# Optimization experiments

Measured on AMD Instinct MI355X. Metric: run time of the kernel, lower is better.

The kernel has to match this reference:

```python
import jax, jax.numpy as jnp
import numpy as np

L = 4          # num_layers
D = 512        # gconv_dim == tlayer_dim
HG, CG = 8, 64 # gconv heads, head dim (D//8)
HT, CT = 4, 128  # tlayer heads, head dim
FF = 4 * D
G, NPG = 128, 256
N = G * NPG
E = N * 16
AF, AV = 9, 64   # atom features / vocab
BF, BV = 3, 8    # bond features / vocab
OUT = 128
SCALE = 0.02


def setup_inputs() -> dict:
    key = jax.random.key(0)
    ks = iter(jax.random.split(key, 64))
    rn = lambda shape: (jax.random.normal(next(ks), shape, dtype=jnp.float32) * SCALE)
    inp = {}
    # float params (stacked over layers)
    inp['atom_emb'] = rn((AF, AV, D))
    inp['bond_emb'] = rn((BF, BV, D))
    for nm in ['gq_w', 'gk_w', 'gv_w', 'ge_w', 'gskip_w', 'mid_w']:
        inp[nm] = rn((L, D, D))
    for nm in ['gq_b', 'gk_b', 'gv_b', 'gskip_b', 'mid_b']:
        inp[nm] = rn((L, D))
    inp['mid_g'] = jnp.ones((L, D), jnp.float32)
    inp['mid_bt'] = jnp.zeros((L, D), jnp.float32)
    for nm in ['tq_w', 'tk_w', 'tv_w', 'to_w']:
        inp[nm] = rn((L, D, D))
    for nm in ['tq_b', 'tk_b', 'tv_b', 'to_b']:
        inp[nm] = rn((L, D))
    inp['ln1_g'] = jnp.ones((L, D), jnp.float32)
    inp['ln1_b'] = jnp.zeros((L, D), jnp.float32)
    inp['f1_w'] = rn((L, D, FF))
    inp['f1_b'] = rn((L, FF))
    inp['f2_w'] = rn((L, FF, D))
    inp['f2_b'] = rn((L, D))
    inp['ln2_g'] = jnp.ones((L, D), jnp.float32)
    inp['ln2_b'] = jnp.zeros((L, D), jnp.float32)
    inp['out_w'] = rn((D, OUT))
    inp['out_b'] = rn((OUT,))
    # int inputs
    inp['x'] = jax.random.randint(next(ks), (N, AF), 0, AV, dtype=jnp.int32)
    inp['edge_attr'] = jax.random.randint(next(ks), (E, BF), 0, BV, dtype=jnp.int32)
    # intra-graph edges: random offsets within each graph
    gid = jax.random.randint(next(ks), (E,), 0, G, dtype=jnp.int32)
    src = gid * NPG + jax.random.randint(next(ks), (E,), 0, NPG, dtype=jnp.int32)
    dst = gid * NPG + jax.random.randint(next(ks), (E,), 0, NPG, dtype=jnp.int32)
    inp['edge_index'] = jnp.stack([src, dst])
    inp['batch'] = jnp.repeat(jnp.arange(G, dtype=jnp.int32), NPG)
    return inp


def _ln(x, g, b, eps=1e-5):
    mu = x.mean(-1, keepdims=True)
    var = ((x - mu) ** 2).mean(-1, keepdims=True)
    return (x - mu) * jax.lax.rsqrt(var + eps) * g + b


def _forward(atom_emb, bond_emb, gq_w, gq_b, gk_w, gk_b, gv_w, gv_b, ge_w,
             gskip_w, gskip_b, mid_w, mid_b, mid_g, mid_bt,
             tq_w, tq_b, tk_w, tk_b, tv_w, tv_b, to_w, to_b,
             ln1_g, ln1_b, f1_w, f1_b, f2_w, f2_b, ln2_g, ln2_b,
             out_w, out_b, x, edge_index, edge_attr, batch):
    # encoders: sum of per-feature embeddings (OGB AtomEncoder/BondEncoder)
    h = atom_emb[jnp.arange(AF)[None, :], x].sum(1)          # [N, D]
    e_attr = bond_emb[jnp.arange(BF)[None, :], edge_attr].sum(1)  # [E, D]
    src, dst = edge_index[0], edge_index[1]

    for i in range(L):
        # --- TransformerConv (PyG): edge-conditioned multi-head graph attention
        q = (h @ gq_w[i] + gq_b[i]).reshape(N, HG, CG)
        k = (h @ gk_w[i] + gk_b[i]).reshape(N, HG, CG)
        v = (h @ gv_w[i] + gv_b[i]).reshape(N, HG, CG)
        ee = (e_attr @ ge_w[i]).reshape(E, HG, CG)           # lin_edge (no bias)
        ke = k[src] + ee
        ve = v[src] + ee
        logits = (q[dst] * ke).sum(-1) / np.sqrt(CG)          # [E, HG]
        m = jax.ops.segment_max(logits, dst, num_segments=N)
        p = jnp.exp(logits - m[dst])
        denom = jax.ops.segment_sum(p, dst, num_segments=N) + 1e-16
        alpha = p / denom[dst]
        agg = jax.ops.segment_sum(alpha[..., None] * ve, dst, num_segments=N)
        h = agg.reshape(N, D) + h @ gskip_w[i] + gskip_b[i]   # root skip
        # --- middle Linear + LayerNorm + ReLU
        h = jax.nn.relu(_ln(h @ mid_w[i] + mid_b[i], mid_g[i], mid_bt[i]))

    xg = h.reshape(G, NPG, D)
    for i in range(L):
        # --- transformer encoder layer, dense attention within each graph
        q = (xg @ tq_w[i] + tq_b[i]).reshape(G, NPG, HT, CT)
        k = (xg @ tk_w[i] + tk_b[i]).reshape(G, NPG, HT, CT)
        v = (xg @ tv_w[i] + tv_b[i]).reshape(G, NPG, HT, CT)
        attn = jax.nn.softmax(jnp.einsum('gqhc,gkhc->ghqk', q, k) / np.sqrt(CT), axis=-1)
        o = jnp.einsum('ghqk,gkhc->gqhc', attn, v).reshape(G, NPG, D)
        xg = _ln(xg + (o @ to_w[i] + to_b[i]), ln1_g[i], ln1_b[i])
        ff = jax.nn.relu(xg @ f1_w[i] + f1_b[i]) @ f2_w[i] + f2_b[i]
        xg = _ln(xg + ff, ln2_g[i], ln2_b[i])

    # mean readout over nodes per graph (segment mean via batch)
    hflat = xg.reshape(N, D)
    cnt = jax.ops.segment_sum(jnp.ones((N,), hflat.dtype), batch, num_segments=G)
    pooled = jax.ops.segment_sum(hflat, batch, num_segments=G) / cnt[:, None]
    return pooled @ out_w + out_b                              # [G, OUT]


def reference(atom_emb, bond_emb, gq_w, gq_b, gk_w, gk_b, gv_w, gv_b, ge_w,
              gskip_w, gskip_b, mid_w, mid_b, mid_g, mid_bt,
              tq_w, tq_b, tk_w, tk_b, tv_w, tv_b, to_w, to_b,
              ln1_g, ln1_b, f1_w, f1_b, f2_w, f2_b, ln2_g, ln2_b,
              out_w, out_b, x, edge_index, edge_attr, batch):
    return _forward(atom_emb, bond_emb, gq_w, gq_b, gk_w, gk_b, gv_w, gv_b, ge_w,
                    gskip_w, gskip_b, mid_w, mid_b, mid_g, mid_bt,
                    tq_w, tq_b, tk_w, tk_b, tv_w, tv_b, to_w, to_b,
                    ln1_g, ln1_b, f1_w, f1_b, f2_w, f2_b, ln2_g, ln2_b,
                    out_w, out_b, x, edge_index, edge_attr, batch)
```

## Files before the change

### kernel.cpp

```cpp
#include <hip/hip_runtime.h>
#include <hip/hip_bf16.h>
#include <math.h>

#define N_NODES 32768
#define DIM     512
#define NE      524288
#define NL      4
#define NG      128
#define NPG_    256
#define HG_     8
#define CG_     64
#define HT_     4
#define CT_     128
#define FF_     2048
#define AF_     9
#define AV_     64
#define BV_     8
#define OUTD    128

typedef unsigned short u16;
typedef __attribute__((ext_vector_type(8))) short bhalf8;
typedef __attribute__((ext_vector_type(4))) float floatx4;
typedef __attribute__((ext_vector_type(8))) unsigned short u16x8;
typedef __attribute__((ext_vector_type(4))) unsigned short u16x4;

__device__ __forceinline__ u16 f2bf(float f) {
  union { float f; unsigned u; } x; x.f = f;
  unsigned r = x.u + 0x7fffu + ((x.u >> 16) & 1u);
  return (u16)(r >> 16);
}
__device__ __forceinline__ float bf2f(u16 u) {
  union { unsigned u; float f; } x; x.u = ((unsigned)u) << 16; return x.f;
}

#define GL2LDS(gp, lp) __builtin_amdgcn_global_load_lds( \
    (const __attribute__((address_space(1))) unsigned int*)(gp), \
    (__attribute__((address_space(3))) unsigned int*)(lp), 16, 0, 0)

__global__ __launch_bounds__(128) void atom_enc_kernel(
    const float* __restrict__ emb, const int* __restrict__ x, u16* __restrict__ hb) {
  int n = blockIdx.x;
  int d4 = threadIdx.x;
  const int* xr = x + n * AF_;
  float4 acc = {0.f, 0.f, 0.f, 0.f};
#pragma unroll
  for (int f = 0; f < AF_; ++f) {
    int idx = xr[f];
    const float4 v = *(const float4*)&emb[((size_t)(f * AV_ + idx)) * DIM + 4 * d4];
    acc.x += v.x; acc.y += v.y; acc.z += v.z; acc.w += v.w;
  }
  u16x4 o;
  o[0] = f2bf(acc.x); o[1] = f2bf(acc.y); o[2] = f2bf(acc.z); o[3] = f2bf(acc.w);
  *(u16x4*)&hb[(size_t)n * DIM + 4 * d4] = o;
}

__global__ __launch_bounds__(512) void bemb_proj_kernel(
    const float* __restrict__ bond_emb, const float* __restrict__ gew, u16* __restrict__ tab) {
  __shared__ float red[8][64];
  int r = blockIdx.x;
  int col = (threadIdx.x & 63) + blockIdx.y * 64;
  int kp = threadIdx.x >> 6;
  const float* a = bond_emb + (size_t)r * DIM + kp * 64;
  const float* w = gew + (size_t)kp * 64 * DIM + col;
  float acc = 0.f;
#pragma unroll 8
  for (int kx = 0; kx < 64; ++kx)
    acc += a[kx] * w[(size_t)kx * DIM];
  red[kp][threadIdx.x & 63] = acc;
  __syncthreads();
  if (threadIdx.x < 64) {
    float s = 0.f;
#pragma unroll
    for (int p = 0; p < 8; ++p) s += red[p][threadIdx.x];
    tab[(size_t)r * DIM + col] = f2bf(s);
  }
}

__global__ __launch_bounds__(256) void wcvt_kernel(
    const float* __restrict__ W, u16* __restrict__ Wt, int K, int N, size_t ostride) {
  __shared__ float t[32][33];
  const size_t mi = (size_t)blockIdx.z * K * N;
  const size_t mo = (size_t)blockIdx.z * ostride;
  int k0 = blockIdx.y * 32, n0 = blockIdx.x * 32;
  int tx = threadIdx.x & 31, ty = threadIdx.x >> 5;
#pragma unroll
  for (int i = 0; i < 32; i += 8)
    t[ty + i][tx] = W[mi + (size_t)(k0 + ty + i) * N + n0 + tx];
  __syncthreads();
#pragma unroll
  for (int i = 0; i < 32; i += 8)
    Wt[mo + (size_t)(n0 + ty + i) * K + k0 + tx] = f2bf(t[tx][ty + i]);
}

__global__ __launch_bounds__(256) void gemm_mfma_kernel(
    const u16* __restrict__ A, const u16* __restrict__ Bt,
    const float* __restrict__ bias, const float* __restrict__ bias1,
    const float* __restrict__ bias2, const float* __restrict__ bias3,
    float* __restrict__ Cf, u16* __restrict__ Cb,
    u16* __restrict__ R1, u16* __restrict__ R2, float* __restrict__ R3f,
    int K, int Nout, int relu, int bf16out, int vtout, int route) {
  __shared__ __align__(16) u16 As[4096];
  __shared__ __align__(16) u16 Bs[4096];
  const int tid = threadIdx.x;
  const int wave = tid >> 6, lane = tid & 63;
  const int bm = blockIdx.y * 128, bn = blockIdx.x * 128;
  const int wr = wave >> 1, wc = wave & 1;

  const size_t rowA = (size_t)bm + (tid >> 2);
  const size_t rowB = (size_t)bn + (tid >> 2);
  const int gofs = (tid & 3) * 8;
  const u16* pA = A + rowA * K + gofs;
  const u16* pB = Bt + rowB * K + gofs;
  u16* lA0 = &As[wave * 512];
  u16* lB0 = &Bs[wave * 512];
  const size_t skip64 = (size_t)64 * K;

  floatx4 acc[4][4] = {};
  const int r = lane & 15, kg = lane >> 4;
  const int aoff = (wr * 64 + r) * 32 + kg * 8;
  const int boff = (wc * 64 + r) * 32 + kg * 8;

  for (int k0 = 0; k0 < K; k0 += 32) {
    GL2LDS(pA + k0, lA0);
    GL2LDS(pA + skip64 + k0, lA0 + 2048);
    GL2LDS(pB + k0, lB0);
    GL2LDS(pB + skip64 + k0, lB0 + 2048);
    __syncthreads();
    bhalf8 af[4], bg[4];
#pragma unroll
    for (int mi = 0; mi < 4; ++mi) af[mi] = *(const bhalf8*)&As[aoff + mi * 512];
#pragma unroll
    for (int ni = 0; ni < 4; ++ni) bg[ni] = *(const bhalf8*)&Bs[boff + ni * 512];
#pragma unroll
    for (int mi = 0; mi < 4; ++mi)
#pragma unroll
      for (int ni = 0; ni < 4; ++ni)
        acc[mi][ni] = __builtin_amdgcn_mfma_f32_16x16x32_bf16(af[mi], bg[ni], acc[mi][ni], 0, 0, 0);
    __syncthreads();
  }

  const int rb = (lane >> 4) * 4;
  const int cc = lane & 15;
  const int seg = (route != 0) ? (bn >> 9) : 0;
  const float* bp = bias;
  if (route != 0) {
    if (seg == 1) bp = bias1;
    else if (seg == 2) bp = bias2;
    else if (seg == 3) bp = bias3;
  }
#pragma unroll
  for (int mi = 0; mi < 4; ++mi) {
#pragma unroll
    for (int ni = 0; ni < 4; ++ni) {
      int gr0 = bm + wr * 64 + mi * 16 + rb;
      int gc = bn + wc * 64 + ni * 16 + cc;
      int c = (route != 0) ? (gc & 511) : gc;
      float bv = bp[c];
#pragma unroll
      for (int reg = 0; reg < 4; ++reg) {
        int gr = gr0 + reg;
        float v = acc[mi][ni][reg] + bv;
        if (relu) v = fmaxf(v, 0.f);
        if (route == 1) {
          size_t idx = (size_t)gr * 512 + c;
          if (seg == 0)      Cb[idx] = f2bf(v);
          else if (seg == 1) R1[idx] = f2bf(v);
          else if (seg == 2) R2[idx] = f2bf(v);
          else               R3f[idx] = v;
        } else if (route == 2) {
          if (seg == 0)      Cb[(size_t)gr * 512 + c] = f2bf(v);
          else if (seg == 1) R1[(size_t)gr * 512 + c] = f2bf(v);
          else               R2[((size_t)(gr >> 8) * DIM + c) * NPG_ + (gr & 255)] = f2bf(v);
        } else if (vtout) {
          Cb[((size_t)(gr >> 8) * DIM + gc) * NPG_ + (gr & 255)] = f2bf(v);
        } else if (bf16out) {
          Cb[(size_t)gr * Nout + gc] = f2bf(v);
        } else {
          Cf[(size_t)gr * Nout + gc] = v;
        }
      }
    }
  }
}

__global__ __launch_bounds__(256) void attn_s_mfma_kernel(
    const u16* __restrict__ q, const u16* __restrict__ k, u16* __restrict__ S, int zbase) {
  __shared__ __align__(16) u16 As[4096];
  __shared__ __align__(16) u16 Bs[4096];
  const int tid = threadIdx.x;
  const int wave = tid >> 6, lane = tid & 63;
  const int zl = blockIdx.z, z = zbase + zl, g = z >> 2, hh = z & 3;
  const int bm = blockIdx.y * 128, bn = blockIdx.x * 128;
  const int wr = wave >> 1, wc = wave & 1;
  const u16* qg = q + (size_t)g * NPG_ * DIM + hh * CT_;
  const u16* kg2 = k + (size_t)g * NPG_ * DIM + hh * CT_;
  const u16* pA = qg + (size_t)(bm + (tid >> 2)) * DIM + (tid & 3) * 8;
  const u16* pB = kg2 + (size_t)(bn + (tid >> 2)) * DIM + (tid & 3) * 8;
  u16* lA0 = &As[wave * 512];
  u16* lB0 = &Bs[wave * 512];
  const size_t skip64 = (size_t)64 * DIM;
  floatx4 acc[4][4] = {};
  const int r = lane & 15, kg_ = lane >> 4;
  const int aoff = (wr * 64 + r) * 32 + kg_ * 8;
  const int boff = (wc * 64 + r) * 32 + kg_ * 8;
  for (int k0 = 0; k0 < CT_; k0 += 32) {
    GL2LDS(pA + k0, lA0);
    GL2LDS(pA + skip64 + k0, lA0 + 2048);
    GL2LDS(pB + k0, lB0);
    GL2LDS(pB + skip64 + k0, lB0 + 2048);
    __syncthreads();
    bhalf8 af[4], bg[4];
#pragma unroll
    for (int mi = 0; mi < 4; ++mi) af[mi] = *(const bhalf8*)&As[aoff + mi * 512];
#pragma unroll
    for (int ni = 0; ni < 4; ++ni) bg[ni] = *(const bhalf8*)&Bs[boff + ni * 512];
#pragma unroll
    for (int mi = 0; mi < 4; ++mi)
#pragma unroll
      for (int ni = 0; ni < 4; ++ni)
        acc[mi][ni] = __builtin_amdgcn_mfma_f32_16x16x32_bf16(af[mi], bg[ni], acc[mi][ni], 0, 0, 0);
    __syncthreads();
  }
  const float sc = 0.08838834764831845f;
  u16* C = S + (size_t)zl * NPG_ * NPG_;
  const int rb = (lane >> 4) * 4, cc = lane & 15;
#pragma unroll
  for (int mi = 0; mi < 4; ++mi)
#pragma unroll
    for (int ni = 0; ni < 4; ++ni) {
      int gr = bm + wr * 64 + mi * 16 + rb;
      int gc = bn + wc * 64 + ni * 16 + cc;
#pragma unroll
      for (int reg = 0; reg < 4; ++reg)
        C[(size_t)(gr + reg) * NPG_ + gc] = f2bf(acc[mi][ni][reg] * sc);
    }
}

__global__ __launch_bounds__(256) void softmax256_kernel(u16* __restrict__ SP) {
  size_t row = (size_t)blockIdx.x * 4 + (threadIdx.x >> 6);
  int lane = threadIdx.x & 63;
  u16* r = SP + row * NPG_;
  u16x4 v = *(u16x4*)&r[lane * 4];
  float x0 = bf2f(v[0]), x1 = bf2f(v[1]), x2 = bf2f(v[2]), x3 = bf2f(v[3]);
  float m = fmaxf(fmaxf(x0, x1), fmaxf(x2, x3));
#pragma unroll
  for (int off = 32; off; off >>= 1) m = fmaxf(m, __shfl_xor(m, off));
  x0 = expf(x0 - m); x1 = expf(x1 - m); x2 = expf(x2 - m); x3 = expf(x3 - m);
  float s = x0 + x1 + x2 + x3;
#pragma unroll
  for (int off = 32; off; off >>= 1) s += __shfl_xor(s, off);
  float inv = 1.0f / s;
  u16x4 o;
  o[0] = f2bf(x0 * inv); o[1] = f2bf(x1 * inv);
  o[2] = f2bf(x2 * inv); o[3] = f2bf(x3 * inv);
  *(u16x4*)&r[lane * 4] = o;
}

__global__ __launch_bounds__(256) void attn_o_mfma_kernel(
    const u16* __restrict__ P, const u16* __restrict__ vt, u16* __restrict__ O, int zbase) {
  __shared__ __align__(16) u16 As[4096];
  __shared__ __align__(16) u16 Bs[4096];
  const int tid = threadIdx.x;
  const int wave = tid >> 6, lane = tid & 63;
  const int zl = blockIdx.z, z = zbase + zl, g = z >> 2, hh = z & 3;
  const int bm = blockIdx.y * 128;
  const int wr = wave >> 1, wc = wave & 1;
  const u16* A = P + (size_t)zl * NPG_ * NPG_;
  const u16* Bt = vt + ((size_t)g * DIM + hh * CT_) * NPG_;
  const u16* pA = A + (size_t)(bm + (tid >> 2)) * NPG_ + (tid & 3) * 8;
  const u16* pB = Bt + (size_t)(tid >> 2) * NPG_ + (tid & 3) * 8;
  u16* lA0 = &As[wave * 512];
  u16* lB0 = &Bs[wave * 512];
  const size_t skip64 = (size_t)64 * NPG_;
  floatx4 acc[4][4] = {};
  const int r = lane & 15, kg_ = lane >> 4;
  const int aoff = (wr * 64 + r) * 32 + kg_ * 8;
  const int boff = (wc * 64 + r) * 32 + kg_ * 8;
  for (int k0 = 0; k0 < NPG_; k0 += 32) {
    GL2LDS(pA + k0, lA0);
    GL2LDS(pA + skip64 + k0, lA0 + 2048);
    GL2LDS(pB + k0, lB0);
    GL2LDS(pB + skip64 + k0, lB0 + 2048);
    __syncthreads();
    bhalf8 af[4], bg[4];
#pragma unroll
    for (int mi = 0; mi < 4; ++mi) af[mi] = *(const bhalf8*)&As[aoff + mi * 512];
#pragma unroll
    for (int ni = 0; ni < 4; ++ni) bg[ni] = *(const bhalf8*)&Bs[boff + ni * 512];
#pragma unroll
    for (int mi = 0; mi < 4; ++mi)
#pragma unroll
      for (int ni = 0; ni < 4; ++ni)
        acc[mi][ni] = __builtin_amdgcn_mfma_f32_16x16x32_bf16(af[mi], bg[ni], acc[mi][ni], 0, 0, 0);
    __syncthreads();
  }
  u16* C = O + ((size_t)g * NPG_) * DIM + hh * CT_;
  const int rb = (lane >> 4) * 4, cc = lane & 15;
#pragma unroll
  for (int mi = 0; mi < 4; ++mi)
#pragma unroll
    for (int ni = 0; ni < 4; ++ni) {
      int gr = bm + wr * 64 + mi * 16 + rb;
      int gc = wc * 64 + ni * 16 + cc;
#pragma unroll
      for (int reg = 0; reg < 4; ++reg)
        C[(size_t)(gr + reg) * DIM + gc] = f2bf(acc[mi][ni][reg]);
    }
}

__global__ __launch_bounds__(256) void gemm_bias_kernel(
    const float* __restrict__ A, const float* __restrict__ W,
    const float* __restrict__ bias, float* __restrict__ C,
    int M, int K, int Nout, int relu) {
  __shared__ float As[16][65];
  __shared__ float Bs[16][64];
  const int bm = blockIdx.y * 64;
  const int bn = blockIdx.x * 64;
  const int tid = threadIdx.x;
  const int tx = tid & 15, ty = tid >> 4;
  float acc[4][4] = {};
  for (int k0 = 0; k0 < K; k0 += 16) {
    {
      int row = tid >> 2;
      int kq = (tid & 3) << 2;
      float4 a = *(const float4*)&A[(size_t)(bm + row) * K + k0 + kq];
      As[kq + 0][row] = a.x; As[kq + 1][row] = a.y; As[kq + 2][row] = a.z; As[kq + 3][row] = a.w;
    }
    {
      int krow = tid >> 4;
      int cq = (tid & 15) << 2;
      *(float4*)&Bs[krow][cq] = *(const float4*)&W[(size_t)(k0 + krow) * Nout + bn + cq];
    }
    __syncthreads();
#pragma unroll
    for (int kk = 0; kk < 16; ++kk) {
      float a[4];
#pragma unroll
      for (int i = 0; i < 4; ++i) a[i] = As[kk][ty * 4 + i];
      float4 b4 = *(const float4*)&Bs[kk][tx * 4];
      float b[4] = {b4.x, b4.y, b4.z, b4.w};
#pragma unroll
      for (int i = 0; i < 4; ++i)
#pragma unroll
        for (int j = 0; j < 4; ++j) acc[i][j] = fmaf(a[i], b[j], acc[i][j]);
    }
    __syncthreads();
  }
  float4 bv = *(const float4*)&bias[bn + tx * 4];
#pragma unroll
  for (int i = 0; i < 4; ++i) {
    int row = bm + ty * 4 + i;
    float4 o;
    o.x = acc[i][0] + bv.x; o.y = acc[i][1] + bv.y;
    o.z = acc[i][2] + bv.z; o.w = acc[i][3] + bv.w;
    if (relu) {
      o.x = fmaxf(o.x, 0.f); o.y = fmaxf(o.y, 0.f);
      o.z = fmaxf(o.z, 0.f); o.w = fmaxf(o.w, 0.f);
    }
    *(float4*)&C[(size_t)row * Nout + bn + tx * 4] = o;
  }
}

__global__ __launch_bounds__(256) void deg_count_kernel(const int* __restrict__ ei, int* __restrict__ deg) {
  int e = blockIdx.x * 256 + threadIdx.x;
  atomicAdd(&deg[ei[NE + e]], 1);
}

__global__ __launch_bounds__(1024) void scan_kernel(const int* __restrict__ deg, int* __restrict__ rp) {
  __shared__ int sums[1024];
  int t = threadIdx.x;
  int base = t * 32;
  int local[32];
  int s = 0;
#pragma unroll
  for (int i = 0; i < 32; ++i) { local[i] = s; s += deg[base + i]; }
  sums[t] = s;
  __syncthreads();
  for (int off = 1; off < 1024; off <<= 1) {
    int other = (t >= off) ? sums[t - off] : 0;
    __syncthreads();
    sums[t] += other;
    __syncthreads();
  }
  int chunk_off = sums[t] - s;
#pragma unroll
  for (int i = 0; i < 32; ++i) rp[base + i] = chunk_off + local[i];
  if (t == 1023) rp[N_NODES] = sums[1023];
}

__global__ __launch_bounds__(256) void scatter_kernel(
    const int* __restrict__ ei, const int* __restrict__ rp,
    int* __restrict__ cur, int* __restrict__ csr) {
  int e = blockIdx.x * 256 + threadIdx.x;
  int d = ei[NE + e];
  int pos = atomicAdd(&cur[d], 1);
  csr[rp[d] + pos] = e;
}

#define CHUNK 128
__global__ __launch_bounds__(512) void edge_agg_kernel(
    const u16* __restrict__ q, const u16* __restrict__ k, const u16* __restrict__ v,
    const u16* __restrict__ tab, const float* __restrict__ skip,
    const int* __restrict__ ei, const int* __restrict__ ea,
    const int* __restrict__ rp, const int* __restrict__ csr, u16* __restrict__ hnew) {
  int n = blockIdx.x;
  int d = threadIdx.x;
  int hh = d >> 6;
  int lane = d & 63;
  int start = rp[n];
  int deg = rp[n + 1] - start;
  __shared__ int s_src[CHUNK];
  __shared__ int s_ea[CHUNK];
  __shared__ float s_p[CHUNK * HG_];
  __shared__ float s_q[DIM];
  __shared__ float s_w[24 * HG_];
  __shared__ float s_max[HG_];
  __shared__ float s_resc[HG_];
  s_q[d] = bf2f(q[(size_t)n * DIM + d]);
  if (d < 24 * HG_) s_w[d] = 0.f;
  if (d < HG_) s_max[d] = -3.0e38f;
  float accum = 0.f, den = 0.f;
  for (int c0 = 0; c0 < deg; c0 += CHUNK) {
    int cnt = min(CHUNK, deg - c0);
    __syncthreads();
    if (d < cnt) {
      int eid = csr[start + c0 + d];
      s_src[d] = ei[eid];
      s_ea[d] = ea[eid * 3] | (ea[eid * 3 + 1] << 8) | (ea[eid * 3 + 2] << 16);
    }
    __syncthreads();
    for (int j = hh; j < cnt; j += 8) {
      int srcn = s_src[j];
      int eap = s_ea[j];
      const u16x8 kv = *(const u16x8*)&k[(size_t)srcn * DIM + lane * 8];
      const size_t to = (size_t)lane * 8;
      const u16x8 e0 = *(const u16x8*)&tab[(size_t)(eap & 0xff) * DIM + to];
      const u16x8 e1 = *(const u16x8*)&tab[(size_t)(8 + ((eap >> 8) & 0xff)) * DIM + to];
      const u16x8 e2 = *(const u16x8*)&tab[(size_t)(16 + (eap >> 16)) * DIM + to];
      float acc = 0.f;
#pragma unroll
      for (int jj = 0; jj < 8; ++jj) {
        float ee = bf2f(e0[jj]) + bf2f(e1[jj]) + bf2f(e2[jj]);
        acc += s_q[lane * 8 + jj] * (bf2f(kv[jj]) + ee);
      }
      acc += __shfl_xor(acc, 1);
      acc += __shfl_xor(acc, 2);
      acc += __shfl_xor(acc, 4);
      if ((lane & 7) == 0) s_p[j * HG_ + (lane >> 3)] = acc * 0.125f;
    }
    __syncthreads();
    float cm = -3.0e38f;
    for (int j = lane; j < cnt; j += 64)
      cm = fmaxf(cm, s_p[j * HG_ + hh]);
#pragma unroll
    for (int off = 32; off; off >>= 1) cm = fmaxf(cm, __shfl_xor(cm, off));
    if (lane == 0) {
      float om = s_max[hh];
      float nm = fmaxf(om, cm);
      s_resc[hh] = (nm > om) ? expf(om - nm) : 1.0f;
      s_max[hh] = nm;
    }
    __syncthreads();
    float rsc = s_resc[hh];
    accum *= rsc;
    den *= rsc;
    if (d < 24 * HG_) s_w[d] *= s_resc[d & 7];
    __syncthreads();
    for (int jh = d; jh < cnt * HG_; jh += 512) {
      int h2 = jh & 7;
      float p = expf(s_p[jh] - s_max[h2]);
      s_p[jh] = p;
      int eap = s_ea[jh >> 3];
      atomicAdd(&s_w[(eap & 0xff) * HG_ + h2], p);
      atomicAdd(&s_w[(8 + ((eap >> 8) & 0xff)) * HG_ + h2], p);
      atomicAdd(&s_w[(16 + (eap >> 16)) * HG_ + h2], p);
    }
    __syncthreads();
    for (int j = 0; j < cnt; ++j) {
      float p = s_p[j * HG_ + hh];
      den += p;
      accum = fmaf(p, bf2f(v[(size_t)s_src[j] * DIM + d]), accum);
    }
  }
  __syncthreads();
#pragma unroll
  for (int r2 = 0; r2 < 24; ++r2)
    accum = fmaf(s_w[r2 * HG_ + hh], bf2f(tab[(size_t)r2 * DIM + d]), accum);
  size_t o = (size_t)n * DIM + d;
  hnew[o] = f2bf(accum / (den + 1e-16f) + skip[o]);
}

__global__ __launch_bounds__(256) void ln_kernel(
    const float* __restrict__ in, const u16* __restrict__ resid,
    const float* __restrict__ g, const float* __restrict__ b,
    u16* __restrict__ outb, int relu) {
  int row = blockIdx.x * 4 + (threadIdx.x >> 6);
  int lane = threadIdx.x & 63;
  size_t base = (size_t)row * DIM + lane * 8;
  float x[8];
  {
    float4 v0 = *(const float4*)&in[base];
    float4 v1 = *(const float4*)&in[base + 4];
    x[0] = v0.x; x[1] = v0.y; x[2] = v0.z; x[3] = v0.w;
    x[4] = v1.x; x[5] = v1.y; x[6] = v1.z; x[7] = v1.w;
  }
  if (resid) {
    u16x8 rv = *(const u16x8*)&resid[base];
#pragma unroll
    for (int i = 0; i < 8; ++i) x[i] += bf2f(rv[i]);
  }
  float s = 0.f;
#pragma unroll
  for (int i = 0; i < 8; ++i) s += x[i];
#pragma unroll
  for (int off = 32; off; off >>= 1) s += __shfl_xor(s, off);
  float mu = s * (1.0f / DIM);
  float vs = 0.f;
#pragma unroll
  for (int i = 0; i < 8; ++i) { float t = x[i] - mu; vs += t * t; }
#pragma unroll
  for (int off = 32; off; off >>= 1) vs += __shfl_xor(vs, off);
  float rstd = 1.0f / sqrtf(vs * (1.0f / DIM) + 1e-5f);
  float4 g0 = *(const float4*)&g[lane * 8];
  float4 g1 = *(const float4*)&g[lane * 8 + 4];
  float4 b0 = *(const float4*)&b[lane * 8];
  float4 b1 = *(const float4*)&b[lane * 8 + 4];
  float gg[8] = {g0.x, g0.y, g0.z, g0.w, g1.x, g1.y, g1.z, g1.w};
  float bb[8] = {b0.x, b0.y, b0.z, b0.w, b1.x, b1.y, b1.z, b1.w};
  u16x8 ob;
#pragma unroll
  for (int i = 0; i < 8; ++i) {
    float y = (x[i] - mu) * rstd * gg[i] + bb[i];
    if (relu) y = fmaxf(y, 0.f);
    ob[i] = f2bf(y);
  }
  *(u16x8*)&outb[base] = ob;
}

__global__ __launch_bounds__(512) void pool_kernel(const u16* __restrict__ xg, float* __restrict__ pooled) {
  int g = blockIdx.x;
  int d = threadIdx.x;
  float acc = 0.f;
  for (int p = 0; p < NPG_; ++p) acc += bf2f(xg[((size_t)g * NPG_ + p) * DIM + d]);
  pooled[(size_t)g * DIM + d] = acc * (1.0f / NPG_);
}

extern "C" void kernel_launch(void* const* d_in, const int* in_sizes, int n_in,
                              void* d_out, int out_size, void* d_ws, size_t ws_size,
                              hipStream_t stream) {
  const float* atom_emb = (const float*)d_in[0];
  const float* bond_emb = (const float*)d_in[1];
  const float* gq_w = (const float*)d_in[2];
  const float* gk_w = (const float*)d_in[3];
  const float* gv_w = (const float*)d_in[4];
  const float* ge_w = (const float*)d_in[5];
  const float* gskip_w = (const float*)d_in[6];
  const float* mid_w = (const float*)d_in[7];
  const float* gq_b = (const float*)d_in[8];
  const float* gk_b = (const float*)d_in[9];
  const float* gv_b = (const float*)d_in[10];
  const float* gskip_b = (const float*)d_in[11];
  const float* mid_b = (const float*)d_in[12];
  const float* mid_g = (const float*)d_in[13];
  const float* mid_bt = (const float*)d_in[14];
  const float* tq_w = (const float*)d_in[15];
  const float* tk_w = (const float*)d_in[16];
  const float* tv_w = (const float*)d_in[17];
  const float* to_w = (const float*)d_in[18];
  const float* tq_b = (const float*)d_in[19];
  const float* tk_b = (const float*)d_in[20];
  const float* tv_b = (const float*)d_in[21];
  const float* to_b = (const float*)d_in[22];
  const float* ln1_g = (const float*)d_in[23];
  const float* ln1_b = (const float*)d_in[24];
  const float* f1_w = (const float*)d_in[25];
  const float* f1_b = (const float*)d_in[26];
  const float* f2_w = (const float*)d_in[27];
  const float* f2_b = (const float*)d_in[28];
  const float* ln2_g = (const float*)d_in[29];
  const float* ln2_b = (const float*)d_in[30];
  const float* out_w = (const float*)d_in[31];
  const float* out_b = (const float*)d_in[32];
  const int* x = (const int*)d_in[33];
  const int* ea = (const int*)d_in[34];
  const int* ei = (const int*)d_in[35];

  char* wbase = (char*)d_ws;
  size_t woff = 0;
  auto ALLOC = [&](size_t bytes) -> void* {
    void* r = wbase + woff;
    woff += (bytes + 255) & ~(size_t)255;
    return r;
  };
  const size_t ND = (size_t)N_NODES * DIM * sizeof(float);
  const size_t NDH = (size_t)N_NODES * DIM * sizeof(u16);
  u16*   wt     = (u16*)ALLOC((size_t)17825792 * sizeof(u16));
  u16*   hb     = (u16*)ALLOC(NDH);
  u16*   Abuf   = (u16*)ALLOC(NDH);
  u16*   Bbuf   = (u16*)ALLOC(NDH);
  u16*   Cbuf   = (u16*)ALLOC(NDH);
  float* E      = (float*)ALLOC(ND);
  u16*   U      = (u16*)ALLOC((size_t)16777216);
  u16*   tab    = (u16*)ALLOC(24 * DIM * sizeof(u16));
  float* pooled = (float*)ALLOC((size_t)NG * DIM * sizeof(float));
  int* deg      = (int*)ALLOC(N_NODES * sizeof(int));
  int* cur      = (int*)ALLOC(N_NODES * sizeof(int));
  int* rp       = (int*)ALLOC((N_NODES + 1) * sizeof(int));
  int* csr      = (int*)ALLOC((size_t)NE * sizeof(int));
  (void)ws_size; (void)in_sizes; (void)n_in; (void)out_size;

  const size_t DD = (size_t)DIM * DIM;
  u16* gfT  = wt;
  u16* midT = wt + 16 * DD;
  u16* tfT  = wt + 20 * DD;
  u16* toT  = wt + 32 * DD;
  u16* f1T  = wt + 36 * DD;
  u16* f2T  = wt + 52 * DD;

  auto wcvt = [&](const float* W, u16* Wt, int K, int N, int L2, size_t ostride) {
    dim3 grid(N / 32, K / 32, L2);
    wcvt_kernel<<<grid, 256, 0, stream>>>(W, Wt, K, N, ostride);
  };
  auto mgemm = [&](const u16* A_, const u16* Bt_, const float* bias_,
                   float* Cf_, u16* Cb_, int M_, int K_, int Nout_,
                   int relu_, int bf16o_, int vtout_) {
    dim3 grid(Nout_ / 128, M_ / 128);
    gemm_mfma_kernel<<<grid, 256, 0, stream>>>(A_, Bt_, bias_, nullptr, nullptr, nullptr,
                                               Cf_, Cb_, nullptr, nullptr, nullptr,
                                               K_, Nout_, relu_, bf16o_, vtout_, 0);
  };

  wcvt(gq_w, gfT + 0 * DD, DIM, DIM, 4, 4 * DD);
  wcvt(gk_w, gfT + 1 * DD, DIM, DIM, 4, 4 * DD);
  wcvt(gv_w, gfT + 2 * DD, DIM, DIM, 4, 4 * DD);
  wcvt(gskip_w, gfT + 3 * DD, DIM, DIM, 4, 4 * DD);
  wcvt(mid_w, midT, DIM, DIM, 4, DD);
  wcvt(tq_w, tfT + 0 * DD, DIM, DIM, 4, 3 * DD);
  wcvt(tk_w, tfT + 1 * DD, DIM, DIM, 4, 3 * DD);
  wcvt(tv_w, tfT + 2 * DD, DIM, DIM, 4, 3 * DD);
  wcvt(to_w, toT, DIM, DIM, 4, DD);
  wcvt(f1_w, f1T, DIM, FF_, 4, 4 * DD);
  wcvt(f2_w, f2T, FF_, DIM, 4, 4 * DD);

  hipMemsetAsync(deg, 0, N_NODES * sizeof(int), stream);
  hipMemsetAsync(cur, 0, N_NODES * sizeof(int), stream);
  deg_count_kernel<<<NE / 256, 256, 0, stream>>>(ei, deg);
  scan_kernel<<<1, 1024, 0, stream>>>(deg, rp);
  scatter_kernel<<<NE / 256, 256, 0, stream>>>(ei, rp, cur, csr);

  atom_enc_kernel<<<N_NODES, 128, 0, stream>>>(atom_emb, x, hb);

  for (int i = 0; i < NL; ++i) {
    bemb_proj_kernel<<<dim3(24, 8), 512, 0, stream>>>(bond_emb, ge_w + i * DD, tab);
    {
      dim3 grid(2048 / 128, N_NODES / 128);
      gemm_mfma_kernel<<<grid, 256, 0, stream>>>(
          hb, gfT + (size_t)i * 4 * DD,
          gq_b + i * DIM, gk_b + i * DIM, gv_b + i * DIM, gskip_b + i * DIM,
          nullptr, Abuf, Bbuf, Cbuf, E,
          DIM, 2048, 0, 0, 0, 1);
    }
    edge_agg_kernel<<<N_NODES, 512, 0, stream>>>(Abuf, Bbuf, Cbuf, tab, E, ei, ea, rp, csr, Abuf);
    mgemm(Abuf, midT + i * DD, mid_b + i * DIM, E, nullptr, N_NODES, DIM, DIM, 0, 0, 0);
    ln_kernel<<<N_NODES / 4, 256, 0, stream>>>(E, nullptr, mid_g + i * DIM, mid_bt + i * DIM, hb, 1);
  }

  for (int i = 0; i < NL; ++i) {
    {
      dim3 grid(1536 / 128, N_NODES / 128);
      gemm_mfma_kernel<<<grid, 256, 0, stream>>>(
          hb, tfT + (size_t)i * 3 * DD,
          tq_b + i * DIM, tk_b + i * DIM, tv_b + i * DIM, nullptr,
          nullptr, Abuf, Bbuf, Cbuf, nullptr,
          DIM, 1536, 0, 0, 0, 2);
    }
    for (int rnd = 0; rnd < 4; ++rnd) {
      attn_s_mfma_kernel<<<dim3(2, 2, 128), 256, 0, stream>>>(Abuf, Bbuf, U, rnd * 128);
      softmax256_kernel<<<(128 * NPG_) / 4, 256, 0, stream>>>(U);
      attn_o_mfma_kernel<<<dim3(1, 2, 128), 256, 0, stream>>>(U, Cbuf, Abuf, rnd * 128);
    }
    mgemm(Abuf, toT + i * DD, to_b + i * DIM, E, nullptr, N_NODES, DIM, DIM, 0, 0, 0);
    ln_kernel<<<N_NODES / 4, 256, 0, stream>>>(E, hb, ln1_g + i * DIM, ln1_b + i * DIM, hb, 0);
    for (int c = 0; c < 4; ++c) {
      mgemm(hb + (size_t)c * 8192 * DIM, f1T + (size_t)i * 4 * DD, f1_b + i * FF_,
            nullptr, Abuf, 8192, DIM, FF_, 1, 1, 0);
      mgemm(Abuf, f2T + (size_t)i * 4 * DD, f2_b + i * DIM,
            E + (size_t)c * 8192 * DIM, nullptr, 8192, FF_, DIM, 0, 0, 0);
    }
    ln_kernel<<<N_NODES / 4, 256, 0, stream>>>(E, hb, ln2_g + i * DIM, ln2_b + i * DIM, hb, 0);
  }

  pool_kernel<<<NG, 512, 0, stream>>>(hb, pooled);
  gemm_bias_kernel<<<dim3(OUTD / 64, NG / 64), 256, 0, stream>>>(pooled, out_w, out_b, (float*)d_out, NG, DIM, OUTD, 0);
}
```

Before: 6.107 ms.

## Split edge logit computation into edge-parallel kernel and compact CSR to u16 arrays

Attention logits for the graph conv are now computed by a separate edge-parallel kernel, one wavefront per edge in CSR order, and written to a float buffer that reuses U. The per-node aggregation kernel only reads those logits, runs the softmax and accumulates V. The scatter step also stores source, destination and packed bond attributes as 16-bit CSR arrays, which removes the indirect edge-id lookups. This aims to raise parallelism and cut the work done by each aggregation block, at the cost of an extra kernel launch and a round trip of the logits through global memory each layer.

```diff
diff --git a/kernel.cpp b/kernel.cpp
--- a/kernel.cpp
+++ b/kernel.cpp
@@ -389,20 +389,50 @@
 }
 
 __global__ __launch_bounds__(256) void scatter_kernel(
-    const int* __restrict__ ei, const int* __restrict__ rp,
-    int* __restrict__ cur, int* __restrict__ csr) {
+    const int* __restrict__ ei, const int* __restrict__ ea, const int* __restrict__ rp,
+    int* __restrict__ cur, u16* __restrict__ csr_src, u16* __restrict__ csr_dst,
+    u16* __restrict__ csr_ea) {
   int e = blockIdx.x * 256 + threadIdx.x;
   int d = ei[NE + e];
   int pos = atomicAdd(&cur[d], 1);
-  csr[rp[d] + pos] = e;
+  int p2 = rp[d] + pos;
+  csr_src[p2] = (u16)ei[e];
+  csr_dst[p2] = (u16)d;
+  csr_ea[p2] = (u16)(ea[e * 3] | (ea[e * 3 + 1] << 4) | (ea[e * 3 + 2] << 8));
+}
+
+__global__ __launch_bounds__(256) void edge_logits_kernel(
+    const u16* __restrict__ q, const u16* __restrict__ k, const u16* __restrict__ tab,
+    const u16* __restrict__ csr_src, const u16* __restrict__ csr_dst,
+    const u16* __restrict__ csr_ea, float* __restrict__ logits) {
+  int e = blockIdx.x * 4 + (threadIdx.x >> 6);
+  int lane = threadIdx.x & 63;
+  int src = csr_src[e], dst = csr_dst[e];
+  int eap = csr_ea[e];
+  int a0 = eap & 15, a1 = (eap >> 4) & 15, a2 = (eap >> 8) & 15;
+  const u16x8 qv = *(const u16x8*)&q[(size_t)dst * DIM + lane * 8];
+  const u16x8 kv = *(const u16x8*)&k[(size_t)src * DIM + lane * 8];
+  const size_t to = (size_t)lane * 8;
+  const u16x8 e0 = *(const u16x8*)&tab[(size_t)a0 * DIM + to];
+  const u16x8 e1 = *(const u16x8*)&tab[(size_t)(8 + a1) * DIM + to];
+  const u16x8 e2 = *(const u16x8*)&tab[(size_t)(16 + a2) * DIM + to];
+  float acc = 0.f;
+#pragma unroll
+  for (int j = 0; j < 8; ++j) {
+    float ee = bf2f(e0[j]) + bf2f(e1[j]) + bf2f(e2[j]);
+    acc += bf2f(qv[j]) * (bf2f(kv[j]) + ee);
+  }
+  acc += __shfl_xor(acc, 1);
+  acc += __shfl_xor(acc, 2);
+  acc += __shfl_xor(acc, 4);
+  if ((lane & 7) == 0) logits[(size_t)e * HG_ + (lane >> 3)] = acc * 0.125f;
 }
 
 #define CHUNK 128
 __global__ __launch_bounds__(512) void edge_agg_kernel(
-    const u16* __restrict__ q, const u16* __restrict__ k, const u16* __restrict__ v,
-    const u16* __restrict__ tab, const float* __restrict__ skip,
-    const int* __restrict__ ei, const int* __restrict__ ea,
-    const int* __restrict__ rp, const int* __restrict__ csr, u16* __restrict__ hnew) {
+    const u16* __restrict__ v, const u16* __restrict__ tab, const float* __restrict__ logits,
+    const float* __restrict__ skip, const u16* __restrict__ csr_src,
+    const u16* __restrict__ csr_ea, const int* __restrict__ rp, u16* __restrict__ hnew) {
   int n = blockIdx.x;
   int d = threadIdx.x;
   int hh = d >> 6;
@@ -412,11 +442,9 @@
   __shared__ int s_src[CHUNK];
   __shared__ int s_ea[CHUNK];
   __shared__ float s_p[CHUNK * HG_];
-  __shared__ float s_q[DIM];
   __shared__ float s_w[24 * HG_];
   __shared__ float s_max[HG_];
   __shared__ float s_resc[HG_];
-  s_q[d] = bf2f(q[(size_t)n * DIM + d]);
   if (d < 24 * HG_) s_w[d] = 0.f;
   if (d < HG_) s_max[d] = -3.0e38f;
   float accum = 0.f, den = 0.f;
@@ -424,30 +452,12 @@
     int cnt = min(CHUNK, deg - c0);
     __syncthreads();
     if (d < cnt) {
-      int eid = csr[start + c0 + d];
-      s_src[d] = ei[eid];
-      s_ea[d] = ea[eid * 3] | (ea[eid * 3 + 1] << 8) | (ea[eid * 3 + 2] << 16);
-    }
-    __syncthreads();
-    for (int j = hh; j < cnt; j += 8) {
-      int srcn = s_src[j];
-      int eap = s_ea[j];
-      const u16x8 kv = *(const u16x8*)&k[(size_t)srcn * DIM + lane * 8];
-      const size_t to = (size_t)lane * 8;
-      const u16x8 e0 = *(const u16x8*)&tab[(size_t)(eap & 0xff) * DIM + to];
-      const u16x8 e1 = *(const u16x8*)&tab[(size_t)(8 + ((eap >> 8) & 0xff)) * DIM + to];
-      const u16x8 e2 = *(const u16x8*)&tab[(size_t)(16 + (eap >> 16)) * DIM + to];
-      float acc = 0.f;
-#pragma unroll
-      for (int jj = 0; jj < 8; ++jj) {
-        float ee = bf2f(e0[jj]) + bf2f(e1[jj]) + bf2f(e2[jj]);
-        acc += s_q[lane * 8 + jj] * (bf2f(kv[jj]) + ee);
-      }
-      acc += __shfl_xor(acc, 1);
-      acc += __shfl_xor(acc, 2);
-      acc += __shfl_xor(acc, 4);
-      if ((lane & 7) == 0) s_p[j * HG_ + (lane >> 3)] = acc * 0.125f;
-    }
+      s_src[d] = csr_src[start + c0 + d];
+      s_ea[d] = csr_ea[start + c0 + d];
+    }
+    __syncthreads();
+    for (int jh = d; jh < cnt * HG_; jh += 512)
+      s_p[jh] = logits[(size_t)(start + c0) * HG_ + jh];
     __syncthreads();
     float cm = -3.0e38f;
     for (int j = lane; j < cnt; j += 64)
@@ -471,9 +481,9 @@
       float p = expf(s_p[jh] - s_max[h2]);
       s_p[jh] = p;
       int eap = s_ea[jh >> 3];
-      atomicAdd(&s_w[(eap & 0xff) * HG_ + h2], p);
-      atomicAdd(&s_w[(8 + ((eap >> 8) & 0xff)) * HG_ + h2], p);
-      atomicAdd(&s_w[(16 + (eap >> 16)) * HG_ + h2], p);
+      atomicAdd(&s_w[(eap & 15) * HG_ + h2], p);
+      atomicAdd(&s_w[(8 + ((eap >> 4) & 15)) * HG_ + h2], p);
+      atomicAdd(&s_w[(16 + ((eap >> 8) & 15)) * HG_ + h2], p);
     }
     __syncthreads();
     for (int j = 0; j < cnt; ++j) {
@@ -606,7 +616,9 @@
   int* deg      = (int*)ALLOC(N_NODES * sizeof(int));
   int* cur      = (int*)ALLOC(N_NODES * sizeof(int));
   int* rp       = (int*)ALLOC((N_NODES + 1) * sizeof(int));
-  int* csr      = (int*)ALLOC((size_t)NE * sizeof(int));
+  u16* csr_src  = (u16*)ALLOC((size_t)NE * sizeof(u16));
+  u16* csr_dst  = (u16*)ALLOC((size_t)NE * sizeof(u16));
+  u16* csr_ea   = (u16*)ALLOC((size_t)NE * sizeof(u16));
   (void)ws_size; (void)in_sizes; (void)n_in; (void)out_size;
 
   const size_t DD = (size_t)DIM * DIM;
@@ -646,7 +658,7 @@
   hipMemsetAsync(cur, 0, N_NODES * sizeof(int), stream);
   deg_count_kernel<<<NE / 256, 256, 0, stream>>>(ei, deg);
   scan_kernel<<<1, 1024, 0, stream>>>(deg, rp);
-  scatter_kernel<<<NE / 256, 256, 0, stream>>>(ei, rp, cur, csr);
+  scatter_kernel<<<NE / 256, 256, 0, stream>>>(ei, ea, rp, cur, csr_src, csr_dst, csr_ea);
 
   atom_enc_kernel<<<N_NODES, 128, 0, stream>>>(atom_emb, x, hb);
 
@@ -660,7 +672,8 @@
           nullptr, Abuf, Bbuf, Cbuf, E,
           DIM, 2048, 0, 0, 0, 1);
     }
-    edge_agg_kernel<<<N_NODES, 512, 0, stream>>>(Abuf, Bbuf, Cbuf, tab, E, ei, ea, rp, csr, Abuf);
+    edge_logits_kernel<<<NE / 4, 256, 0, stream>>>(Abuf, Bbuf, tab, csr_src, csr_dst, csr_ea, (float*)U);
+    edge_agg_kernel<<<N_NODES, 512, 0, stream>>>(Cbuf, tab, (float*)U, E, csr_src, csr_ea, rp, Abuf);
     mgemm(Abuf, midT + i * DD, mid_b + i * DIM, E, nullptr, N_NODES, DIM, DIM, 0, 0, 0);
     ln_kernel<<<N_NODES / 4, 256, 0, stream>>>(E, nullptr, mid_g + i * DIM, mid_bt + i * DIM, hb, 1);
   }
```

Result: no change. 6.126 ms (+0.3%).
